# Kernel tuning notes

Hardware: AMD Instinct MI355X
Metric: run time of the kernel (lower is better)

## Reference

```python
import jax, jax.numpy as jnp
import numpy as np

D_MODEL = 1024
NUM_HEADS = 16
HEAD_DIM = D_MODEL // NUM_HEADS  # 64
MAX_SEQ_LEN = 2048
BASE = 10000.0


def _rope_tables(seq_len):
    # theta_i = base^(-2i/hd) for i in [0, hd/2)
    theta = 1.0 / (BASE ** (jnp.arange(0, HEAD_DIM, 2, dtype=jnp.float32) / HEAD_DIM))
    angles = jnp.arange(seq_len, dtype=jnp.float32)[:, None] * theta  # [S, hd/2]
    return jnp.cos(angles), jnp.sin(angles)


def _apply_rope(x, cos, sin):
    # x: [B, H, S, hd]; cos/sin: [S, hd/2] broadcast over B,H
    x1 = x[..., 0::2]
    x2 = x[..., 1::2]
    r1 = x1 * cos - x2 * sin
    r2 = x1 * sin + x2 * cos
    return jnp.stack([r1, r2], axis=-1).reshape(x.shape)  # interleave back


def setup_inputs() -> dict:
    key = jax.random.key(0)
    k_x, k_q, k_k, k_v, k_o = jax.random.split(key, 5)
    B, S = 2, 2048
    x = jax.random.normal(k_x, (B, S, D_MODEL), dtype=jnp.float32)
    init = 0.02
    w_q = jax.random.normal(k_q, (D_MODEL, D_MODEL), dtype=jnp.float32) * init
    w_k = jax.random.normal(k_k, (D_MODEL, D_MODEL), dtype=jnp.float32) * init
    w_v = jax.random.normal(k_v, (D_MODEL, D_MODEL), dtype=jnp.float32) * init
    w_o = jax.random.normal(k_o, (D_MODEL, D_MODEL), dtype=jnp.float32) * init
    return {"x": x, "w_q": w_q, "w_k": w_k, "w_v": w_v, "w_o": w_o}


def reference(x, w_q, w_k, w_v, w_o):
    # Prefill path: start_pos=0, cache=None, eval-mode dropout (identity).
    B, S, D = x.shape
    H, hd = NUM_HEADS, HEAD_DIM
    scale = 1.0 / (hd ** 0.5)

    # nn.Linear(bias=False): y = x @ W.T
    q = (x @ w_q.T).reshape(B, S, H, hd).transpose(0, 2, 1, 3)  # [B,H,S,hd]
    k = (x @ w_k.T).reshape(B, S, H, hd).transpose(0, 2, 1, 3)
    v = (x @ w_v.T).reshape(B, S, H, hd).transpose(0, 2, 1, 3)

    cos, sin = _rope_tables(S)  # same tables for every head (per-head torch loop vectorized)
    q_rot = _apply_rope(q, cos, sin)
    k_rot = _apply_rope(k, cos, sin)

    attn = jnp.einsum("bhqd,bhkd->bhqk", q_rot, k_rot) * scale  # [B,H,S,S]
    # causal mask: triu(ones(S,S), diagonal = S_k - S_q + 1 = 1)
    causal = jnp.triu(jnp.ones((S, S), dtype=bool), k=1)
    attn = jnp.where(causal[None, None], -jnp.inf, attn)
    attn_w = jax.nn.softmax(attn, axis=-1)

    out = jnp.einsum("bhqk,bhkd->bhqd", attn_w, v)  # [B,H,S,hd]
    out = out.transpose(0, 2, 1, 3).reshape(B, S, D)
    return out @ w_o.T
```

## Files before the change

### kernel.cpp

```cpp
#include <hip/hip_runtime.h>
#include <hip/hip_bf16.h>
#include <math.h>


#define S_LEN 2048
#define NHEADS 16
#define HD 64
#define DM 1024

typedef __attribute__((ext_vector_type(8))) short bf16x8;
typedef __attribute__((ext_vector_type(4))) float f32x4;

#define MFMA16(a, b, c) __builtin_amdgcn_mfma_f32_16x16x32_bf16((a), (b), (c), 0, 0, 0)
#define NEG_BIG (-1e30f)

#define GLOAD_LDS16(g, l)                                                      \
    __builtin_amdgcn_global_load_lds(                                          \
        (const __attribute__((address_space(1))) void*)(g),                    \
        (__attribute__((address_space(3))) void*)(l), 16, 0, 0)

__global__ __launch_bounds__(256) void convert_kernel(
    const float* __restrict__ x,  const float* __restrict__ wq,
    const float* __restrict__ wk, const float* __restrict__ wv,
    const float* __restrict__ wo,
    __hip_bfloat16* __restrict__ xb,  __hip_bfloat16* __restrict__ wqb,
    __hip_bfloat16* __restrict__ wkb, __hip_bfloat16* __restrict__ wvb,
    __hip_bfloat16* __restrict__ wob, float2* __restrict__ tab)
{
    const int y = blockIdx.y;
    if (y == 8) {
        const int gid = blockIdx.x * 256 + threadIdx.x;
        if (gid < S_LEN * 32) {
            const int s = gid >> 5, p = gid & 31;
            float theta = powf(10000.0f, -(float)(2 * p) * (1.0f / 64.0f));
            float sn, cs;
            sincosf((float)s * theta, &sn, &cs);
            tab[gid] = make_float2(cs, sn);
        }
        return;
    }
    const float* src;
    __hip_bfloat16* dst;
    size_t off = 0;
    if (y < 4)      { src = x;  dst = xb;  off = (size_t)y * 1048576; }
    else if (y == 4) { src = wq; dst = wqb; }
    else if (y == 5) { src = wk; dst = wkb; }
    else if (y == 6) { src = wv; dst = wvb; }
    else             { src = wo; dst = wob; }

    const size_t i = off + ((size_t)blockIdx.x * 256 + threadIdx.x) * 4;
    float4 v = *(const float4*)(src + i);
    __hip_bfloat16 t[4] = { __float2bfloat16(v.x), __float2bfloat16(v.y),
                            __float2bfloat16(v.z), __float2bfloat16(v.w) };
    *(ushort4*)(dst + i) = *(ushort4*)t;
}

__global__ __launch_bounds__(256) void qkv_kernel(
    const __hip_bfloat16* __restrict__ X,
    const __hip_bfloat16* __restrict__ Wq,
    const __hip_bfloat16* __restrict__ Wk,
    const __hip_bfloat16* __restrict__ Wv,
    __hip_bfloat16* __restrict__ qws,
    __hip_bfloat16* __restrict__ kws,
    __hip_bfloat16* __restrict__ vws)
{
    const int z = blockIdx.z;
    const __hip_bfloat16* __restrict__ W = (z == 0) ? Wq : (z == 1) ? Wk : Wv;
    __hip_bfloat16* __restrict__ out = (z == 0) ? qws : (z == 1) ? kws : vws;

    __shared__ __align__(16) __hip_bfloat16 Asm[128 * 32];
    __shared__ __align__(16) __hip_bfloat16 Bsm[128 * 32];

    const int tid = threadIdx.x;
    const int wave = tid >> 6, lane = tid & 63;
    const int quad = lane >> 4, l15 = lane & 15;
    const int wm = (wave >> 1) * 64, wn = (wave & 1) * 64;
    const int m0 = blockIdx.y * 128, n0 = blockIdx.x * 128;

    f32x4 acc[4][4] = {};

    for (int k0 = 0; k0 < DM; k0 += 32) {
#pragma unroll
        for (int c = 0; c < 2; c++) {
            int idx = c * 2048 + tid * 8;
            int r = idx >> 5, kc = idx & 31;
            GLOAD_LDS16(X + (size_t)(m0 + r) * DM + k0 + kc, &Asm[idx]);
            GLOAD_LDS16(W + (size_t)(n0 + r) * DM + k0 + kc, &Bsm[idx]);
        }
        __syncthreads();
        bf16x8 af[4], bfv[4];
#pragma unroll
        for (int i = 0; i < 4; i++)
            af[i] = *(const bf16x8*)(&Asm[(wm + i * 16 + l15) * 32 + quad * 8]);
#pragma unroll
        for (int j = 0; j < 4; j++)
            bfv[j] = *(const bf16x8*)(&Bsm[(wn + j * 16 + l15) * 32 + quad * 8]);
#pragma unroll
        for (int i = 0; i < 4; i++)
#pragma unroll
            for (int j = 0; j < 4; j++)
                acc[i][j] = MFMA16(af[i], bfv[j], acc[i][j]);
        __syncthreads();
    }

#pragma unroll
    for (int i = 0; i < 4; i++) {
#pragma unroll
        for (int r = 0; r < 4; r++) {
            int m = m0 + wm + i * 16 + quad * 4 + r;
            int b = m >> 11, s = m & 2047;
#pragma unroll
            for (int j = 0; j < 4; j++) {
                int col = n0 + wn + j * 16 + l15;
                int h = col >> 6, d = col & 63;
                size_t idx = (z == 2)
                    ? (((size_t)(b * NHEADS + h)) * HD + d) * S_LEN + s
                    : (((size_t)(b * NHEADS + h)) * S_LEN + s) * HD + d;
                out[idx] = __float2bfloat16(acc[i][j][r]);
            }
        }
    }
}

__global__ __launch_bounds__(256) void rope_kernel(
    __hip_bfloat16* __restrict__ q, __hip_bfloat16* __restrict__ k,
    const float2* __restrict__ tab)
{
    __hip_bfloat16* __restrict__ p = (blockIdx.y == 0) ? q : k;
    const float qscale = (blockIdx.y == 0) ? 0.18033688011112042f
                                           : 1.0f;
    const int gid = blockIdx.x * 256 + threadIdx.x;
    const int e0 = gid * 8;
    const int s = (gid >> 3) & 2047;
    const int p4 = (gid & 7) * 4;

    const float2* tp = tab + s * 32 + p4;
    float4 t01 = *(const float4*)(tp);
    float4 t23 = *(const float4*)(tp + 2);
    float cs[4] = { t01.x, t01.z, t23.x, t23.z };
    float sn[4] = { t01.y, t01.w, t23.y, t23.w };

    int4 raw = *(const int4*)(p + e0);
    __hip_bfloat16* v = (__hip_bfloat16*)&raw;
#pragma unroll
    for (int i = 0; i < 4; i++) {
        float x1 = __bfloat162float(v[2 * i]);
        float x2 = __bfloat162float(v[2 * i + 1]);
        v[2 * i]     = __float2bfloat16((x1 * cs[i] - x2 * sn[i]) * qscale);
        v[2 * i + 1] = __float2bfloat16((x1 * sn[i] + x2 * cs[i]) * qscale);
    }
    *(int4*)(p + e0) = raw;
}


#define SMPV(sc, mm, ll, oo, Pr)                                               \
    do {                                                                       \
        float pm[4];                                                           \
        _Pragma("unroll")                                                      \
        for (int r = 0; r < 4; r++)                                            \
            pm[r] = fmaxf(fmaxf(sc[0][r], sc[1][r]),                           \
                          fmaxf(sc[2][r], sc[3][r]));                          \
        bool ok = true;                                                        \
        _Pragma("unroll")                                                      \
        for (int r = 0; r < 4; r++) ok = ok && (pm[r] <= mm[r] + 11.0f);       \
        if (!__all(ok)) {                                                      \
            _Pragma("unroll")                                                  \
            for (int off = 1; off < 16; off <<= 1)                             \
                _Pragma("unroll")                                              \
                for (int r = 0; r < 4; r++)                                    \
                    pm[r] = fmaxf(pm[r], __shfl_xor(pm[r], off));              \
            _Pragma("unroll")                                                  \
            for (int r = 0; r < 4; r++) {                                      \
                float mn = fmaxf(mm[r], pm[r]);                                \
                float al = exp2f(mm[r] - mn);                                  \
                mm[r] = mn;                                                    \
                ll[r] *= al;                                                   \
                _Pragma("unroll")                                              \
                for (int t = 0; t < 4; t++) oo[t][r] *= al;                    \
            }                                                                  \
        }                                                                      \
        _Pragma("unroll")                                                      \
        for (int t = 0; t < 4; t++)                                            \
            _Pragma("unroll")                                                  \
            for (int r = 0; r < 4; r++)                                        \
                Pr[(quad * 4 + r) * 72 + t * 16 + l15] =                       \
                    __float2bfloat16(exp2f(sc[t][r] - mm[r]));                 \
        _Pragma("unroll")                                                      \
        for (int st = 0; st < 2; st++) {                                       \
            bf16x8 pf = *(const bf16x8*)(&Pr[l15 * 72 + st * 32 + quad * 8]);  \
            __builtin_amdgcn_s_setprio(1);                                     \
            ll = MFMA16(pf, ones, ll);                                         \
            _Pragma("unroll")                                                  \
            for (int t = 0; t < 4; t++) oo[t] = MFMA16(pf, vf[st][t], oo[t]);  \
            __builtin_amdgcn_s_setprio(0);                                     \
        }                                                                      \
    } while (0)

#define LOAD_VF(kv0)                                                           \
    do {                                                                       \
        _Pragma("unroll")                                                      \
        for (int st = 0; st < 2; st++)                                         \
            _Pragma("unroll")                                                  \
            for (int t = 0; t < 4; t++)                                        \
                vf[st][t] = *(const bf16x8*)(Vtb +                             \
                    (size_t)(t * 16 + l15) * S_LEN + (kv0) + st * 32 + quad * 8); \
    } while (0)

#define LOAD_KF(kv0)                                                           \
    do {                                                                       \
        _Pragma("unroll")                                                      \
        for (int st = 0; st < 2; st++)                                         \
            _Pragma("unroll")                                                  \
            for (int t = 0; t < 4; t++)                                        \
                kf[st][t] = *(const bf16x8*)(Kb +                              \
                    (size_t)((kv0) + t * 16 + l15) * HD + st * 32 + quad * 8); \
    } while (0)

#define QK(sc, qf)                                                             \
    do {                                                                       \
        __builtin_amdgcn_s_setprio(1);                                         \
        _Pragma("unroll")                                                      \
        for (int st = 0; st < 2; st++)                                         \
            _Pragma("unroll")                                                  \
            for (int t = 0; t < 4; t++) sc[t] = MFMA16(qf[st], kf[st][t], sc[t]); \
        __builtin_amdgcn_s_setprio(0);                                         \
    } while (0)

#define MASK(sc, rowbase, kv0)                                                 \
    do {                                                                       \
        _Pragma("unroll")                                                      \
        for (int t = 0; t < 4; t++) {                                          \
            int col = (kv0) + t * 16 + l15;                                    \
            _Pragma("unroll")                                                  \
            for (int r = 0; r < 4; r++) {                                      \
                int row = (rowbase) + quad * 4 + r;                            \
                if (col > row) sc[t][r] = NEG_BIG;                             \
            }                                                                  \
        }                                                                      \
    } while (0)

__global__ __launch_bounds__(256) void attn_kernel(
    const __hip_bfloat16* __restrict__ Qg,
    const __hip_bfloat16* __restrict__ Kg,
    const __hip_bfloat16* __restrict__ Vtg,
    __hip_bfloat16* __restrict__ Og)
{
    const int bh = blockIdx.x;
    const int qi = (blockIdx.y < 8) ? blockIdx.y : 23 - blockIdx.y;
    const int tid = threadIdx.x;
    const int w = tid >> 6, lane = tid & 63;
    const int quad = lane >> 4, l15 = lane & 15;
    const size_t base = (size_t)bh * S_LEN * HD;
    const __hip_bfloat16* Qb = Qg + base;
    const __hip_bfloat16* Kb = Kg + base;
    const __hip_bfloat16* Vtb = Vtg + base;
    const int b = bh >> 4, h = bh & 15;

    __shared__ __align__(16) __hip_bfloat16 Pl[128 * 72];
    __hip_bfloat16* PrA = &Pl[w * 32 * 72];
    __hip_bfloat16* PrB = PrA + 16 * 72;

    const int q0 = qi * 128;
    const int rowA = q0 + w * 16;
    const int rowB = rowA + 64;

    bf16x8 qfA[2], qfB[2];
#pragma unroll
    for (int st = 0; st < 2; st++) {
        qfA[st] = *(const bf16x8*)(Qb + (size_t)(rowA + l15) * HD + st * 32 + quad * 8);
        qfB[st] = *(const bf16x8*)(Qb + (size_t)(rowB + l15) * HD + st * 32 + quad * 8);
    }

    bf16x8 ones;
#pragma unroll
    for (int i = 0; i < 8; i++) ones[i] = (short)0x3F80;

    float mA[4], mB[4];
    f32x4 lA = {}, lB = {};
    f32x4 oA[4] = {}, oB[4] = {};
#pragma unroll
    for (int r = 0; r < 4; r++) { mA[r] = NEG_BIG; mB[r] = NEG_BIG; }

    bf16x8 kf[2][4];
    bf16x8 vf[2][4];
    LOAD_KF(0);

#pragma unroll 1
    for (int j = 0; j < 2 * qi; j++) {
        const int kv0 = j * 64;
        LOAD_VF(kv0);
        f32x4 scA[4] = {}, scB[4] = {};
        QK(scA, qfA);
        QK(scB, qfB);
        LOAD_KF(kv0 + 64);
        SMPV(scA, mA, lA, oA, PrA);
        SMPV(scB, mB, lB, oB, PrB);
    }

    {
        const int kv0 = q0;
        LOAD_VF(kv0);
        f32x4 scA[4] = {}, scB[4] = {};
        QK(scA, qfA);
        QK(scB, qfB);
        LOAD_KF(kv0 + 64);
        MASK(scA, rowA, kv0);
        SMPV(scA, mA, lA, oA, PrA);
        SMPV(scB, mB, lB, oB, PrB);
    }

    {
        const int kv0 = q0 + 64;
        LOAD_VF(kv0);
        f32x4 scB[4] = {};
        QK(scB, qfB);
        MASK(scB, rowB, kv0);
        SMPV(scB, mB, lB, oB, PrB);
    }

#pragma unroll
    for (int t = 0; t < 4; t++)
#pragma unroll
        for (int r = 0; r < 4; r++) {
            int d = t * 16 + l15;
            int sA = rowA + quad * 4 + r;
            Og[((size_t)(b * S_LEN + sA)) * DM + h * HD + d] =
                __float2bfloat16(oA[t][r] / lA[r]);
            int sB = rowB + quad * 4 + r;
            Og[((size_t)(b * S_LEN + sB)) * DM + h * HD + d] =
                __float2bfloat16(oB[t][r] / lB[r]);
        }
}

__global__ __launch_bounds__(256) void oproj_kernel(
    const __hip_bfloat16* __restrict__ A,
    const __hip_bfloat16* __restrict__ W,
    float* __restrict__ out)
{
    __shared__ __align__(16) __hip_bfloat16 Asm[128 * 32];
    __shared__ __align__(16) __hip_bfloat16 Bsm[128 * 32];

    const int tid = threadIdx.x;
    const int wave = tid >> 6, lane = tid & 63;
    const int quad = lane >> 4, l15 = lane & 15;
    const int wm = (wave >> 1) * 64, wn = (wave & 1) * 64;
    const int m0 = blockIdx.y * 128, n0 = blockIdx.x * 128;

    f32x4 acc[4][4] = {};

    for (int k0 = 0; k0 < DM; k0 += 32) {
#pragma unroll
        for (int c = 0; c < 2; c++) {
            int idx = c * 2048 + tid * 8;
            int r = idx >> 5, kc = idx & 31;
            GLOAD_LDS16(A + (size_t)(m0 + r) * DM + k0 + kc, &Asm[idx]);
            GLOAD_LDS16(W + (size_t)(n0 + r) * DM + k0 + kc, &Bsm[idx]);
        }
        __syncthreads();
        bf16x8 af[4], bfv[4];
#pragma unroll
        for (int i = 0; i < 4; i++)
            af[i] = *(const bf16x8*)(&Asm[(wm + i * 16 + l15) * 32 + quad * 8]);
#pragma unroll
        for (int j = 0; j < 4; j++)
            bfv[j] = *(const bf16x8*)(&Bsm[(wn + j * 16 + l15) * 32 + quad * 8]);
#pragma unroll
        for (int i = 0; i < 4; i++)
#pragma unroll
            for (int j = 0; j < 4; j++)
                acc[i][j] = MFMA16(af[i], bfv[j], acc[i][j]);
        __syncthreads();
    }

#pragma unroll
    for (int i = 0; i < 4; i++)
#pragma unroll
        for (int r = 0; r < 4; r++) {
            int m = m0 + wm + i * 16 + quad * 4 + r;
#pragma unroll
            for (int j = 0; j < 4; j++) {
                int col = n0 + wn + j * 16 + l15;
                __hip_bfloat16 bb = __float2bfloat16(acc[i][j][r]);
                unsigned int u = ((unsigned int)(*(unsigned short*)&bb)) << 16;
                out[(size_t)m * DM + col] = __uint_as_float(u);
            }
        }
}

extern "C" void kernel_launch(void* const* d_in, const int* in_sizes, int n_in,
                              void* d_out, int out_size, void* d_ws, size_t ws_size,
                              hipStream_t stream)
{
    const float* x  = (const float*)d_in[0];
    const float* wq = (const float*)d_in[1];
    const float* wk = (const float*)d_in[2];
    const float* wv = (const float*)d_in[3];
    const float* wo = (const float*)d_in[4];
    float* out = (float*)d_out;

    const size_t xe = (size_t)2 * S_LEN * DM;
    const size_t we = (size_t)DM * DM;
    __hip_bfloat16* xb  = (__hip_bfloat16*)d_ws;
    __hip_bfloat16* wqb = xb + xe;
    __hip_bfloat16* wkb = wqb + we;
    __hip_bfloat16* wvb = wkb + we;
    __hip_bfloat16* wob = wvb + we;
    __hip_bfloat16* qws = wob + we;
    __hip_bfloat16* kws = qws + xe;
    __hip_bfloat16* vws = kws + xe;
    __hip_bfloat16* aws = vws + xe;
    float2* tab = (float2*)aws;

    dim3 blk(256, 1, 1);
    convert_kernel<<<dim3(1024, 9, 1), blk, 0, stream>>>(x, wq, wk, wv, wo,
                                                         xb, wqb, wkb, wvb, wob, tab);
    qkv_kernel<<<dim3(8, 32, 3), blk, 0, stream>>>(xb, wqb, wkb, wvb, qws, kws, vws);
    rope_kernel<<<dim3(2048, 2, 1), blk, 0, stream>>>(qws, kws, tab);
    attn_kernel<<<dim3(32, 16, 1), blk, 0, stream>>>(qws, kws, vws, aws);
    oproj_kernel<<<dim3(8, 32, 1), blk, 0, stream>>>(aws, wob, out);
}
```

Before: 216.2 us.

## Fuse RoPE into QKV epilogue, rebalance causal attention rows, use native exp2

Applies RoPE and the Q softmax scale inside the QKV GEMM epilogue, pairing adjacent columns with a lane shuffle. This removes the separate rope kernel launch and its extra read/write pass over Q and K. Attention now gives each wave a pair of 16-row strips, one from the top and one mirrored from the bottom of the causal triangle, handled in a single loop, so every wave does similar work. exp2f is swapped for the hardware exp2 builtin, which may differ slightly in precision.

```diff
diff --git a/kernel.cpp b/kernel.cpp
--- a/kernel.cpp
+++ b/kernel.cpp
@@ -13,6 +13,12 @@
 
 #define MFMA16(a, b, c) __builtin_amdgcn_mfma_f32_16x16x32_bf16((a), (b), (c), 0, 0, 0)
 #define NEG_BIG (-1e30f)
+
+#if __has_builtin(__builtin_amdgcn_exp2f)
+#define EXP2F(x) __builtin_amdgcn_exp2f(x)
+#else
+#define EXP2F(x) exp2f(x)
+#endif
 
 #define GLOAD_LDS16(g, l)                                                      \
     __builtin_amdgcn_global_load_lds(                                          \
@@ -62,11 +68,14 @@
     const __hip_bfloat16* __restrict__ Wv,
     __hip_bfloat16* __restrict__ qws,
     __hip_bfloat16* __restrict__ kws,
-    __hip_bfloat16* __restrict__ vws)
+    __hip_bfloat16* __restrict__ vws,
+    const float2* __restrict__ tab)
 {
     const int z = blockIdx.z;
     const __hip_bfloat16* __restrict__ W = (z == 0) ? Wq : (z == 1) ? Wk : Wv;
     __hip_bfloat16* __restrict__ out = (z == 0) ? qws : (z == 1) ? kws : vws;
+    const float qkscale = (z == 0) ? 0.18033688011112042f
+                                   : 1.0f;
 
     __shared__ __align__(16) __hip_bfloat16 Asm[128 * 32];
     __shared__ __align__(16) __hip_bfloat16 Bsm[128 * 32];
@@ -103,6 +112,7 @@
         __syncthreads();
     }
 
+    const bool odd = (l15 & 1);
 #pragma unroll
     for (int i = 0; i < 4; i++) {
 #pragma unroll
@@ -113,43 +123,23 @@
             for (int j = 0; j < 4; j++) {
                 int col = n0 + wn + j * 16 + l15;
                 int h = col >> 6, d = col & 63;
+                float v = acc[i][j][r];
+                if (z < 2) {
+                    float other = __shfl_xor(v, 1);
+                    float2 t = tab[s * 32 + (d >> 1)];
+                    float x1 = odd ? other : v;
+                    float x2 = odd ? v : other;
+                    v = odd ? (x1 * t.y + x2 * t.x)
+                            : (x1 * t.x - x2 * t.y);
+                    v *= qkscale;
+                }
                 size_t idx = (z == 2)
                     ? (((size_t)(b * NHEADS + h)) * HD + d) * S_LEN + s
                     : (((size_t)(b * NHEADS + h)) * S_LEN + s) * HD + d;
-                out[idx] = __float2bfloat16(acc[i][j][r]);
+                out[idx] = __float2bfloat16(v);
             }
         }
     }
-}
-
-__global__ __launch_bounds__(256) void rope_kernel(
-    __hip_bfloat16* __restrict__ q, __hip_bfloat16* __restrict__ k,
-    const float2* __restrict__ tab)
-{
-    __hip_bfloat16* __restrict__ p = (blockIdx.y == 0) ? q : k;
-    const float qscale = (blockIdx.y == 0) ? 0.18033688011112042f
-                                           : 1.0f;
-    const int gid = blockIdx.x * 256 + threadIdx.x;
-    const int e0 = gid * 8;
-    const int s = (gid >> 3) & 2047;
-    const int p4 = (gid & 7) * 4;
-
-    const float2* tp = tab + s * 32 + p4;
-    float4 t01 = *(const float4*)(tp);
-    float4 t23 = *(const float4*)(tp + 2);
-    float cs[4] = { t01.x, t01.z, t23.x, t23.z };
-    float sn[4] = { t01.y, t01.w, t23.y, t23.w };
-
-    int4 raw = *(const int4*)(p + e0);
-    __hip_bfloat16* v = (__hip_bfloat16*)&raw;
-#pragma unroll
-    for (int i = 0; i < 4; i++) {
-        float x1 = __bfloat162float(v[2 * i]);
-        float x2 = __bfloat162float(v[2 * i + 1]);
-        v[2 * i]     = __float2bfloat16((x1 * cs[i] - x2 * sn[i]) * qscale);
-        v[2 * i + 1] = __float2bfloat16((x1 * sn[i] + x2 * cs[i]) * qscale);
-    }
-    *(int4*)(p + e0) = raw;
 }
 
 
@@ -172,7 +162,7 @@
             _Pragma("unroll")                                                  \
             for (int r = 0; r < 4; r++) {                                      \
                 float mn = fmaxf(mm[r], pm[r]);                                \
-                float al = exp2f(mm[r] - mn);                                  \
+                float al = EXP2F(mm[r] - mn);                                  \
                 mm[r] = mn;                                                    \
                 ll[r] *= al;                                                   \
                 _Pragma("unroll")                                              \
@@ -184,7 +174,7 @@
             _Pragma("unroll")                                                  \
             for (int r = 0; r < 4; r++)                                        \
                 Pr[(quad * 4 + r) * 72 + t * 16 + l15] =                       \
-                    __float2bfloat16(exp2f(sc[t][r] - mm[r]));                 \
+                    __float2bfloat16(EXP2F(sc[t][r] - mm[r]));                 \
         _Pragma("unroll")                                                      \
         for (int st = 0; st < 2; st++) {                                       \
             bf16x8 pf = *(const bf16x8*)(&Pr[l15 * 72 + st * 32 + quad * 8]);  \
@@ -246,7 +236,6 @@
     __hip_bfloat16* __restrict__ Og)
 {
     const int bh = blockIdx.x;
-    const int qi = (blockIdx.y < 8) ? blockIdx.y : 23 - blockIdx.y;
     const int tid = threadIdx.x;
     const int w = tid >> 6, lane = tid & 63;
     const int quad = lane >> 4, l15 = lane & 15;
@@ -260,9 +249,11 @@
     __hip_bfloat16* PrA = &Pl[w * 32 * 72];
     __hip_bfloat16* PrB = PrA + 16 * 72;
 
-    const int q0 = qi * 128;
-    const int rowA = q0 + w * 16;
-    const int rowB = rowA + 64;
+    const int a = blockIdx.y * 4 + w;
+    const int rowA = a * 16;
+    const int rowB = 2032 - a * 16;
+    const int jA = a >> 2;
+    const int jB = 31 - jA;
 
     bf16x8 qfA[2], qfB[2];
 #pragma unroll
@@ -286,35 +277,22 @@
     LOAD_KF(0);
 
 #pragma unroll 1
-    for (int j = 0; j < 2 * qi; j++) {
+    for (int j = 0; j <= jB; j++) {
         const int kv0 = j * 64;
+        const bool aact = (j <= jA);
+
         LOAD_VF(kv0);
+
         f32x4 scA[4] = {}, scB[4] = {};
-        QK(scA, qfA);
         QK(scB, qfB);
-        LOAD_KF(kv0 + 64);
-        SMPV(scA, mA, lA, oA, PrA);
-        SMPV(scB, mB, lB, oB, PrB);
-    }
-
-    {
-        const int kv0 = q0;
-        LOAD_VF(kv0);
-        f32x4 scA[4] = {}, scB[4] = {};
-        QK(scA, qfA);
-        QK(scB, qfB);
-        LOAD_KF(kv0 + 64);
-        MASK(scA, rowA, kv0);
-        SMPV(scA, mA, lA, oA, PrA);
-        SMPV(scB, mB, lB, oB, PrB);
-    }
-
-    {
-        const int kv0 = q0 + 64;
-        LOAD_VF(kv0);
-        f32x4 scB[4] = {};
-        QK(scB, qfB);
-        MASK(scB, rowB, kv0);
+        if (aact) QK(scA, qfA);
+
+        if (j < jB) LOAD_KF(kv0 + 64);
+
+        if (j == jA) MASK(scA, rowA, kv0);
+        if (j == jB) MASK(scB, rowB, kv0);
+
+        if (aact) SMPV(scA, mA, lA, oA, PrA);
         SMPV(scB, mB, lB, oB, PrB);
     }
 
@@ -414,8 +392,8 @@
     dim3 blk(256, 1, 1);
     convert_kernel<<<dim3(1024, 9, 1), blk, 0, stream>>>(x, wq, wk, wv, wo,
                                                          xb, wqb, wkb, wvb, wob, tab);
-    qkv_kernel<<<dim3(8, 32, 3), blk, 0, stream>>>(xb, wqb, wkb, wvb, qws, kws, vws);
-    rope_kernel<<<dim3(2048, 2, 1), blk, 0, stream>>>(qws, kws, tab);
+    qkv_kernel<<<dim3(8, 32, 3), blk, 0, stream>>>(xb, wqb, wkb, wvb,
+                                                   qws, kws, vws, tab);
     attn_kernel<<<dim3(32, 16, 1), blk, 0, stream>>>(qws, kws, vws, aws);
     oproj_kernel<<<dim3(8, 32, 1), blk, 0, stream>>>(aws, wob, out);
 }
```

Result: slower. 274.1 us (+26.8%).
